# Optimization experiments

Hardware: AMD Instinct MI355X
Metric: run time of the kernel (lower is better)

Reference implementation:

```python
import jax, jax.numpy as jnp
import numpy as np

EPS = 1e-6
DELTA = 1e-6
GAMMA = 1.0


def setup_inputs() -> dict:
    key = jax.random.key(0)
    ks = jax.random.split(key, 6)
    B, N, D, DDIR, DSIM = 2, 384, 256, 128, 64
    sc = lambda d: 1.0 / np.sqrt(d)
    return {
        "t": jax.random.normal(ks[0], (B, N, D), jnp.float32),
        "Qd": jax.random.normal(ks[1], (D, DDIR), jnp.float32) * sc(D),
        "Kd": jax.random.normal(ks[2], (D, DDIR), jnp.float32) * sc(D),
        "Vd": jax.random.normal(ks[3], (DDIR, D), jnp.float32) * sc(DDIR),
        "Qs": jax.random.normal(ks[4], (D, DSIM), jnp.float32) * sc(D),
        "Ks": jax.random.normal(ks[5], (D, DSIM), jnp.float32) * sc(D),
        "a_l": jnp.ones((1,), jnp.float32),
        "b_l": jnp.zeros((1,), jnp.float32),
    }


def reference(t, Qd, Kd, Vd, Qs, Ks, a_l, b_l):
    B, N, D = t.shape
    d_sim = Qs.shape[1]
    # --- similarity: s_ij = <Qs t_i, Ks t_j>/sqrt(d_sim), then symmetrize ---
    q = t @ Qs  # (B,N,d_sim)
    k = t @ Ks
    s = jnp.einsum('bnd,bmd->bnm', q, k) / jnp.sqrt(jnp.float32(d_sim))
    s = 0.5 * (s + s.transpose(0, 2, 1))
    # --- global z-score over off-diagonal entries (biased var) ---
    eye = jnp.eye(N, dtype=bool)[None]  # (1,N,N)
    cnt = jnp.float32(N * (N - 1))
    mu = jnp.where(eye, 0.0, s).sum((1, 2), keepdims=True) / cnt  # (B,1,1)
    var = jnp.where(eye, 0.0, (s - mu) ** 2).sum((1, 2), keepdims=True) / cnt
    s_hat = (s - mu) / jnp.sqrt(var + EPS)
    tilde_s = a_l.reshape(-1, 1, 1) * s_hat + b_l.reshape(-1, 1, 1)
    # --- gates / mass / inertia / apportioned step ---
    A = jax.nn.sigmoid(tilde_s)                                  # (B,N,N)
    m = 1.0 / (jnp.exp(GAMMA * tilde_s).sum(axis=2) + EPS)       # (B,N)
    w = A * m[:, None, :]                                        # w_ij = m_j A_ij
    alpha = A * (w / (w.sum(axis=2, keepdims=True) + DELTA))     # (B,N,N)
    # --- antisymmetric Hadamard direction gate ---
    qd = t @ Qd  # (B,N,d_dir)
    kd = t @ Kd
    had = qd[:, :, None, :] * kd[:, None, :, :]                  # (B,N,N,d_dir)
    kappa = jnp.einsum('bijr,rd->bijd', had, Vd)                 # (B,N,N,D)
    gate = jax.nn.sigmoid(kappa - kappa.transpose(0, 2, 1, 3))
    Dpair = gate * (t[:, :, None, :] - t[:, None, :, :])         # D_ij = gate*(t_i - t_j)
    # --- exclude self pairs, aggregate update ---
    off = ~eye  # (1,N,N)
    alpha = jnp.where(off, alpha, 0.0)
    Dpair = jnp.where(off[..., None], Dpair, 0.0)
    t_next = t - jnp.einsum('bnm,bnmd->bnd', alpha, Dpair)
    return t_next
```

## Files before the change

### kernel.cpp

```cpp
#include <hip/hip_runtime.h>

#define Bn 2
#define Nn 384
#define Dn 256
#define Rn 128
#define Sn 64
#define BNn (Bn*Nn)

typedef short short8 __attribute__((ext_vector_type(8)));
typedef float f32x4 __attribute__((ext_vector_type(4)));
typedef unsigned int uint;
typedef unsigned short ushort;

static __device__ __forceinline__ float fast_sigmoid(float x) {
    return __builtin_amdgcn_rcpf(1.0f + __expf(-x));
}

static __device__ __forceinline__ ushort f2bf(float f) {
    uint u = __float_as_uint(f);
    uint r = (u + 0x7fffu + ((u >> 16) & 1u)) >> 16;
    return (ushort)r;
}
static __device__ __forceinline__ float bf2f(ushort u) {
    return __uint_as_float(((uint)u) << 16);
}

__global__ void zero_stats(float* __restrict__ stats) {
    if (threadIdx.x < 8) stats[threadIdx.x] = 0.0f;
}

__global__ void proj_kernel(const float* __restrict__ t,
                            const float* __restrict__ Qd, const float* __restrict__ Kd,
                            const float* __restrict__ Qs, const float* __restrict__ Ks,
                            float* __restrict__ q, float* __restrict__ k,
                            ushort* __restrict__ qdb, ushort* __restrict__ kdb) {
    __shared__ float trow[4][Dn];
    const int r0 = blockIdx.x * 4;
    const int tid = threadIdx.x;
    for (int idx = tid; idx < 4 * Dn; idx += 384)
        trow[idx >> 8][idx & 255] = t[(size_t)(r0 + (idx >> 8)) * Dn + (idx & 255)];
    __syncthreads();
    const float* W;
    float* of = nullptr;
    ushort* ob = nullptr;
    int ncol, col;
    if (tid < 64)       { W = Qs; of = q;   ncol = 64;  col = tid; }
    else if (tid < 128) { W = Ks; of = k;   ncol = 64;  col = tid - 64; }
    else if (tid < 256) { W = Qd; ob = qdb; ncol = 128; col = tid - 128; }
    else                { W = Kd; ob = kdb; ncol = 128; col = tid - 256; }
    float a0 = 0.f, a1 = 0.f, a2 = 0.f, a3 = 0.f;
    for (int kk = 0; kk < Dn; kk += 4) {
        float4 t0 = *(const float4*)&trow[0][kk];
        float4 t1 = *(const float4*)&trow[1][kk];
        float4 t2 = *(const float4*)&trow[2][kk];
        float4 t3 = *(const float4*)&trow[3][kk];
        float w0 = W[(size_t)(kk + 0) * ncol + col];
        float w1 = W[(size_t)(kk + 1) * ncol + col];
        float w2 = W[(size_t)(kk + 2) * ncol + col];
        float w3 = W[(size_t)(kk + 3) * ncol + col];
        a0 += t0.x * w0 + t0.y * w1 + t0.z * w2 + t0.w * w3;
        a1 += t1.x * w0 + t1.y * w1 + t1.z * w2 + t1.w * w3;
        a2 += t2.x * w0 + t2.y * w1 + t2.z * w2 + t2.w * w3;
        a3 += t3.x * w0 + t3.y * w1 + t3.z * w2 + t3.w * w3;
    }
    if (of) {
        of[(size_t)(r0 + 0) * ncol + col] = a0;
        of[(size_t)(r0 + 1) * ncol + col] = a1;
        of[(size_t)(r0 + 2) * ncol + col] = a2;
        of[(size_t)(r0 + 3) * ncol + col] = a3;
    } else {
        ob[(size_t)(r0 + 0) * ncol + col] = f2bf(a0);
        ob[(size_t)(r0 + 1) * ncol + col] = f2bf(a1);
        ob[(size_t)(r0 + 2) * ncol + col] = f2bf(a2);
        ob[(size_t)(r0 + 3) * ncol + col] = f2bf(a3);
    }
}

__global__ void prep_vdt(const float* __restrict__ Vd, ushort* __restrict__ VdT) {
    const int idx = blockIdx.x * 256 + threadIdx.x;
    const int d = idx >> 7, r = idx & 127;
    VdT[idx] = f2bf(Vd[(size_t)r * Dn + d]);
}

__global__ void ssym_kernel(const float* __restrict__ q, const float* __restrict__ k,
                            float* __restrict__ ssym, float* __restrict__ stats) {
    __shared__ float qi[16][68], ki[16][68], qj[16][68], kj[16][68];
    __shared__ float red[256];
    const int b = blockIdx.z, it = blockIdx.x, jt = blockIdx.y;
    const int tid = threadIdx.x;
    const int r0 = tid >> 6, c = tid & 63;
#pragma unroll
    for (int p = 0; p < 4; ++p) {
        int row = r0 + 4 * p;
        qi[row][c] = q[((size_t)(b * Nn + it * 16 + row)) * Sn + c];
        ki[row][c] = k[((size_t)(b * Nn + it * 16 + row)) * Sn + c];
        qj[row][c] = q[((size_t)(b * Nn + jt * 16 + row)) * Sn + c];
        kj[row][c] = k[((size_t)(b * Nn + jt * 16 + row)) * Sn + c];
    }
    __syncthreads();
    const int ti = tid >> 4, tj = tid & 15;
    float acc = 0.0f;
#pragma unroll
    for (int dd = 0; dd < Sn; dd += 4) {
        float4 a  = *(const float4*)&qi[ti][dd];
        float4 bb = *(const float4*)&kj[tj][dd];
        float4 cc = *(const float4*)&qj[tj][dd];
        float4 d  = *(const float4*)&ki[ti][dd];
        acc += a.x * bb.x + a.y * bb.y + a.z * bb.z + a.w * bb.w
             + cc.x * d.x + cc.y * d.y + cc.z * d.z + cc.w * d.w;
    }
    const float sval = acc * 0.0625f;
    const int gi = it * 16 + ti, gj = jt * 16 + tj;
    ssym[((size_t)(b * Nn + gi)) * Nn + gj] = sval;
    const float v = (gi == gj) ? 0.0f : sval;

    red[tid] = v;
    __syncthreads();
    for (int off = 128; off > 0; off >>= 1) {
        if (tid < off) red[tid] += red[tid + off];
        __syncthreads();
    }
    const float tot_s = red[0];
    __syncthreads();
    red[tid] = v * v;
    __syncthreads();
    for (int off = 128; off > 0; off >>= 1) {
        if (tid < off) red[tid] += red[tid + off];
        __syncthreads();
    }
    if (tid == 0) {
        atomicAdd(&stats[b * 2 + 0], tot_s);
        atomicAdd(&stats[b * 2 + 1], red[0]);
    }
}

__global__ void stats_fin(float* __restrict__ stats) {
    const int b = threadIdx.x;
    if (b < Bn) {
        const float cnt = (float)(Nn * (Nn - 1));
        const float mu = stats[b * 2 + 0] / cnt;
        const float var = stats[b * 2 + 1] / cnt - mu * mu;
        stats[4 + b * 2 + 0] = mu;
        stats[4 + b * 2 + 1] = rsqrtf(var + 1e-6f);
    }
}

__global__ void m_kernel(const float* __restrict__ ssym, const float* __restrict__ stats,
                         const float* __restrict__ a_l, const float* __restrict__ b_l,
                         float* __restrict__ m) {
    const int row = blockIdx.x;
    const int b = row / Nn;
    const float mu = stats[4 + b * 2], isg = stats[5 + b * 2];
    const float a = a_l[0], bb = b_l[0];
    const int tid = threadIdx.x;
    float sum = 0.0f;
    for (int j = tid; j < Nn; j += 128) {
        float til = a * (ssym[(size_t)row * Nn + j] - mu) * isg + bb;
        sum += __expf(til);
    }
    __shared__ float red[128];
    red[tid] = sum;
    __syncthreads();
    for (int off = 64; off > 0; off >>= 1) {
        if (tid < off) red[tid] += red[tid + off];
        __syncthreads();
    }
    if (tid == 0) m[row] = 1.0f / (red[0] + 1e-6f);
}

__global__ void alpha_kernel(const float* __restrict__ ssym, const float* __restrict__ stats,
                             const float* __restrict__ a_l, const float* __restrict__ b_l,
                             const float* __restrict__ m, float* __restrict__ alpha) {
    const int row = blockIdx.x;
    const int b = row / Nn;
    const int i = row - b * Nn;
    const float mu = stats[4 + b * 2], isg = stats[5 + b * 2];
    const float a = a_l[0], bb = b_l[0];
    const int tid = threadIdx.x;
    float wsum = 0.0f;
    for (int j = tid; j < Nn; j += 128) {
        float til = a * (ssym[(size_t)row * Nn + j] - mu) * isg + bb;
        float A = fast_sigmoid(til);
        wsum += A * m[b * Nn + j];
    }
    __shared__ float red[128];
    red[tid] = wsum;
    __syncthreads();
    for (int off = 64; off > 0; off >>= 1) {
        if (tid < off) red[tid] += red[tid + off];
        __syncthreads();
    }
    const float inv = 1.0f / (red[0] + 1e-6f);
    for (int j = tid; j < Nn; j += 128) {
        float til = a * (ssym[(size_t)row * Nn + j] - mu) * isg + bb;
        float A = fast_sigmoid(til);
        float al = A * A * m[b * Nn + j] * inv;
        alpha[(size_t)row * Nn + j] = (j == i) ? 0.0f : al;
    }
}

__global__ __launch_bounds__(256, 3)
void pair_kernel(const float* __restrict__ t, const ushort* __restrict__ qdb,
                 const ushort* __restrict__ kdb, const ushort* __restrict__ VdT,
                 const float* __restrict__ alpha, float* __restrict__ out) {
    __shared__ ushort h_s[128][136];
    __shared__ float alpha_s[Nn];
    __shared__ float qdi_s[Rn], kdi_s[Rn];

    const int bi = blockIdx.x;
    const int b = bi / Nn;
    const int tid = threadIdx.x;
    const int wave = tid >> 6, lane = tid & 63;
    const int ln = lane & 15, quad = lane >> 4;
    const int wd0 = wave * 64;

    for (int idx = tid; idx < Nn; idx += 256) alpha_s[idx] = alpha[(size_t)bi * Nn + idx];
    if (tid < Rn) {
        qdi_s[tid] = bf2f(qdb[(size_t)bi * Rn + tid]);
        kdi_s[tid] = bf2f(kdb[(size_t)bi * Rn + tid]);
    }

    short8 vf[4][4];
#pragma unroll
    for (int dt = 0; dt < 4; ++dt)
#pragma unroll
        for (int ks = 0; ks < 4; ++ks)
            vf[dt][ks] = *(const short8*)&VdT[(size_t)(wd0 + dt * 16 + ln) * Rn + ks * 32 + quad * 8];

    float4 tiv[4];
#pragma unroll
    for (int dt = 0; dt < 4; ++dt)
        tiv[dt] = *(const float4*)&t[(size_t)bi * Dn + wd0 + dt * 16 + quad * 4];

    float4 outac[4];
#pragma unroll
    for (int dt = 0; dt < 4; ++dt) outac[dt] = make_float4(0.f, 0.f, 0.f, 0.f);

    __syncthreads();

    for (int jt0 = 0; jt0 < Nn; jt0 += 128) {
        {
            const int jj = tid >> 1;
            const int r0 = (tid & 1) * 64;
            const size_t rowj = (size_t)(b * Nn + jt0 + jj) * Rn;
            const uint4* qp = (const uint4*)(qdb + rowj + r0);
            const uint4* kp = (const uint4*)(kdb + rowj + r0);
#pragma unroll
            for (int c = 0; c < 8; ++c) {
                uint4 qv = qp[c], kv = kp[c];
                uint pk[4];
#pragma unroll
                for (int p = 0; p < 4; ++p) {
                    uint qu = (&qv.x)[p], ku = (&kv.x)[p];
                    float qlo = __uint_as_float(qu << 16);
                    float qhi = __uint_as_float(qu & 0xffff0000u);
                    float klo = __uint_as_float(ku << 16);
                    float khi = __uint_as_float(ku & 0xffff0000u);
                    const int r = r0 + c * 8 + p * 2;
                    float h0 = qdi_s[r]     * klo - kdi_s[r]     * qlo;
                    float h1 = qdi_s[r + 1] * khi - kdi_s[r + 1] * qhi;
                    pk[p] = (uint)f2bf(h0) | ((uint)f2bf(h1) << 16);
                }
                uint4 w; w.x = pk[0]; w.y = pk[1]; w.z = pk[2]; w.w = pk[3];
                *(uint4*)&h_s[jj][r0 + c * 8] = w;
            }
        }
        __syncthreads();

#pragma unroll 1
        for (int jsub = 0; jsub < 8; ++jsub) {
            short8 hf[4];
#pragma unroll
            for (int ks = 0; ks < 4; ++ks)
                hf[ks] = *(const short8*)&h_s[jsub * 16 + ln][ks * 32 + quad * 8];
            const int j = jt0 + jsub * 16 + ln;
            const float al = alpha_s[j];
            const size_t trow = (size_t)(b * Nn + j) * Dn;
#pragma unroll
            for (int dt = 0; dt < 4; ++dt) {
                float4 tj = *(const float4*)&t[trow + wd0 + dt * 16 + quad * 4];
                f32x4 acc = {0.f, 0.f, 0.f, 0.f};
#pragma unroll
                for (int ks = 0; ks < 4; ++ks)
                    acc = __builtin_amdgcn_mfma_f32_16x16x32_bf16(vf[dt][ks], hf[ks], acc, 0, 0, 0);
                outac[dt].x += al * fast_sigmoid(acc[0]) * (tiv[dt].x - tj.x);
                outac[dt].y += al * fast_sigmoid(acc[1]) * (tiv[dt].y - tj.y);
                outac[dt].z += al * fast_sigmoid(acc[2]) * (tiv[dt].z - tj.z);
                outac[dt].w += al * fast_sigmoid(acc[3]) * (tiv[dt].w - tj.w);
            }
        }
        __syncthreads();
    }

#pragma unroll
    for (int dt = 0; dt < 4; ++dt) {
        float4 v = outac[dt];
#pragma unroll
        for (int mask = 1; mask < 16; mask <<= 1) {
            v.x += __shfl_xor(v.x, mask);
            v.y += __shfl_xor(v.y, mask);
            v.z += __shfl_xor(v.z, mask);
            v.w += __shfl_xor(v.w, mask);
        }
        if (ln == 0) {
            float4 o;
            o.x = tiv[dt].x - v.x;
            o.y = tiv[dt].y - v.y;
            o.z = tiv[dt].z - v.z;
            o.w = tiv[dt].w - v.w;
            *(float4*)&out[(size_t)bi * Dn + wd0 + dt * 16 + quad * 4] = o;
        }
    }
}

extern "C" void kernel_launch(void* const* d_in, const int* in_sizes, int n_in,
                              void* d_out, int out_size, void* d_ws, size_t ws_size,
                              hipStream_t stream) {
    const float* t   = (const float*)d_in[0];
    const float* Qd  = (const float*)d_in[1];
    const float* Kd  = (const float*)d_in[2];
    const float* Vd  = (const float*)d_in[3];
    const float* Qs  = (const float*)d_in[4];
    const float* Ks  = (const float*)d_in[5];
    const float* a_l = (const float*)d_in[6];
    const float* b_l = (const float*)d_in[7];
    float* out = (float*)d_out;
    float* ws  = (float*)d_ws;

    float* q     = ws;
    float* k     = q + BNn * Sn;
    float* ssym  = k + BNn * Sn;
    float* alpha = ssym + (size_t)BNn * Nn;
    float* m     = alpha + (size_t)BNn * Nn;
    float* stats = m + BNn;
    ushort* qdb  = (ushort*)(stats + 8);
    ushort* kdb  = qdb + (size_t)BNn * Rn;
    ushort* VdT  = kdb + (size_t)BNn * Rn;

    hipLaunchKernelGGL(zero_stats, dim3(1), dim3(64), 0, stream, stats);
    hipLaunchKernelGGL(proj_kernel, dim3(BNn / 4), dim3(384), 0, stream,
                       t, Qd, Kd, Qs, Ks, q, k, qdb, kdb);
    hipLaunchKernelGGL(prep_vdt, dim3(128), dim3(256), 0, stream, Vd, VdT);
    hipLaunchKernelGGL(ssym_kernel, dim3(Nn / 16, Nn / 16, Bn), dim3(256), 0, stream,
                       q, k, ssym, stats);
    hipLaunchKernelGGL(stats_fin, dim3(1), dim3(64), 0, stream, stats);
    hipLaunchKernelGGL(m_kernel, dim3(BNn), dim3(128), 0, stream, ssym, stats, a_l, b_l, m);
    hipLaunchKernelGGL(alpha_kernel, dim3(BNn), dim3(128), 0, stream, ssym, stats, a_l, b_l, m, alpha);
    hipLaunchKernelGGL(pair_kernel, dim3(BNn), dim3(256), 0, stream,
                       t, qdb, kdb, VdT, alpha, out);
}
```

Measured before the change: 197.7 us.

## Fuse prep and alpha kernels, fold log2e into Vd, split MFMA chains

Merges the stats zeroing, projection and Vd transpose kernels into one prep kernel, and folds the stats finalisation and alpha computation into the m and pair kernels. This cuts the launch count and drops the alpha buffer round-trip through global memory. It also pre-scales VdT by -log2(e) so the gate sigmoid uses exp2 directly. In the pair kernel, t_j loads are hoisted ahead of the MFMAs and the dependent MFMA chain is split into two independent accumulators. In exchange, every pair block recomputes its alpha row and the stats finalisation.

```diff
diff --git a/kernel.cpp b/kernel.cpp
--- a/kernel.cpp
+++ b/kernel.cpp
@@ -6,6 +6,7 @@
 #define Rn 128
 #define Sn 64
 #define BNn (Bn*Nn)
+#define NEG_LOG2E -1.44269504088896f
 
 typedef short short8 __attribute__((ext_vector_type(8)));
 typedef float f32x4 __attribute__((ext_vector_type(4)));
@@ -15,7 +16,6 @@
 static __device__ __forceinline__ float fast_sigmoid(float x) {
     return __builtin_amdgcn_rcpf(1.0f + __expf(-x));
 }
-
 static __device__ __forceinline__ ushort f2bf(float f) {
     uint u = __float_as_uint(f);
     uint r = (u + 0x7fffu + ((u >> 16) & 1u)) >> 16;
@@ -25,65 +25,81 @@
     return __uint_as_float(((uint)u) << 16);
 }
 
-__global__ void zero_stats(float* __restrict__ stats) {
-    if (threadIdx.x < 8) stats[threadIdx.x] = 0.0f;
-}
-
-__global__ void proj_kernel(const float* __restrict__ t,
-                            const float* __restrict__ Qd, const float* __restrict__ Kd,
-                            const float* __restrict__ Qs, const float* __restrict__ Ks,
-                            float* __restrict__ q, float* __restrict__ k,
-                            ushort* __restrict__ qdb, ushort* __restrict__ kdb) {
+__global__ __launch_bounds__(256)
+void prep_kernel(const float* __restrict__ t,
+                 const float* __restrict__ Qd, const float* __restrict__ Kd,
+                 const float* __restrict__ Vd,
+                 const float* __restrict__ Qs, const float* __restrict__ Ks,
+                 float* __restrict__ q, float* __restrict__ k,
+                 ushort* __restrict__ qdb, ushort* __restrict__ kdb,
+                 ushort* __restrict__ VdT, float* __restrict__ stats) {
+    const int bi = blockIdx.x;
+    const int tid = threadIdx.x;
+    if (bi >= 192) {
+        const int idx = (bi - 192) * 256 + tid;
+        const int d = idx >> 7, r = idx & 127;
+        VdT[idx] = f2bf(NEG_LOG2E * Vd[(size_t)r * Dn + d]);
+        if (bi == 319 && tid < 4) stats[tid] = 0.0f;
+        return;
+    }
     __shared__ float trow[4][Dn];
-    const int r0 = blockIdx.x * 4;
-    const int tid = threadIdx.x;
-    for (int idx = tid; idx < 4 * Dn; idx += 384)
-        trow[idx >> 8][idx & 255] = t[(size_t)(r0 + (idx >> 8)) * Dn + (idx & 255)];
-    __syncthreads();
-    const float* W;
-    float* of = nullptr;
-    ushort* ob = nullptr;
-    int ncol, col;
-    if (tid < 64)       { W = Qs; of = q;   ncol = 64;  col = tid; }
-    else if (tid < 128) { W = Ks; of = k;   ncol = 64;  col = tid - 64; }
-    else if (tid < 256) { W = Qd; ob = qdb; ncol = 128; col = tid - 128; }
-    else                { W = Kd; ob = kdb; ncol = 128; col = tid - 256; }
-    float a0 = 0.f, a1 = 0.f, a2 = 0.f, a3 = 0.f;
-    for (int kk = 0; kk < Dn; kk += 4) {
-        float4 t0 = *(const float4*)&trow[0][kk];
-        float4 t1 = *(const float4*)&trow[1][kk];
-        float4 t2 = *(const float4*)&trow[2][kk];
-        float4 t3 = *(const float4*)&trow[3][kk];
-        float w0 = W[(size_t)(kk + 0) * ncol + col];
-        float w1 = W[(size_t)(kk + 1) * ncol + col];
-        float w2 = W[(size_t)(kk + 2) * ncol + col];
-        float w3 = W[(size_t)(kk + 3) * ncol + col];
-        a0 += t0.x * w0 + t0.y * w1 + t0.z * w2 + t0.w * w3;
-        a1 += t1.x * w0 + t1.y * w1 + t1.z * w2 + t1.w * w3;
-        a2 += t2.x * w0 + t2.y * w1 + t2.z * w2 + t2.w * w3;
-        a3 += t3.x * w0 + t3.y * w1 + t3.z * w2 + t3.w * w3;
-    }
-    if (of) {
-        of[(size_t)(r0 + 0) * ncol + col] = a0;
-        of[(size_t)(r0 + 1) * ncol + col] = a1;
-        of[(size_t)(r0 + 2) * ncol + col] = a2;
-        of[(size_t)(r0 + 3) * ncol + col] = a3;
-    } else {
-        ob[(size_t)(r0 + 0) * ncol + col] = f2bf(a0);
-        ob[(size_t)(r0 + 1) * ncol + col] = f2bf(a1);
-        ob[(size_t)(r0 + 2) * ncol + col] = f2bf(a2);
-        ob[(size_t)(r0 + 3) * ncol + col] = f2bf(a3);
-    }
-}
-
-__global__ void prep_vdt(const float* __restrict__ Vd, ushort* __restrict__ VdT) {
-    const int idx = blockIdx.x * 256 + threadIdx.x;
-    const int d = idx >> 7, r = idx & 127;
-    VdT[idx] = f2bf(Vd[(size_t)r * Dn + d]);
-}
-
-__global__ void ssym_kernel(const float* __restrict__ q, const float* __restrict__ k,
-                            float* __restrict__ ssym, float* __restrict__ stats) {
+    const int r0 = bi * 4;
+    for (int idx = tid; idx < 4 * Dn; idx += 256)
+        trow[idx >> 8][idx & 255] = t[(size_t)r0 * Dn + idx];
+    __syncthreads();
+    {
+        const float* W = (tid < 128) ? Qd : Kd;
+        ushort* ob = (tid < 128) ? qdb : kdb;
+        const int col = tid & 127;
+        float a0 = 0.f, a1 = 0.f, a2 = 0.f, a3 = 0.f;
+        for (int kk = 0; kk < Dn; kk += 4) {
+            float4 t0 = *(const float4*)&trow[0][kk];
+            float4 t1 = *(const float4*)&trow[1][kk];
+            float4 t2 = *(const float4*)&trow[2][kk];
+            float4 t3 = *(const float4*)&trow[3][kk];
+            float w0 = W[(size_t)(kk + 0) * 128 + col];
+            float w1 = W[(size_t)(kk + 1) * 128 + col];
+            float w2 = W[(size_t)(kk + 2) * 128 + col];
+            float w3 = W[(size_t)(kk + 3) * 128 + col];
+            a0 += t0.x * w0 + t0.y * w1 + t0.z * w2 + t0.w * w3;
+            a1 += t1.x * w0 + t1.y * w1 + t1.z * w2 + t1.w * w3;
+            a2 += t2.x * w0 + t2.y * w1 + t2.z * w2 + t2.w * w3;
+            a3 += t3.x * w0 + t3.y * w1 + t3.z * w2 + t3.w * w3;
+        }
+        ob[(size_t)(r0 + 0) * 128 + col] = f2bf(a0);
+        ob[(size_t)(r0 + 1) * 128 + col] = f2bf(a1);
+        ob[(size_t)(r0 + 2) * 128 + col] = f2bf(a2);
+        ob[(size_t)(r0 + 3) * 128 + col] = f2bf(a3);
+    }
+    if (tid < 128) {
+        const float* W = (tid < 64) ? Qs : Ks;
+        float* of = (tid < 64) ? q : k;
+        const int col = tid & 63;
+        float a0 = 0.f, a1 = 0.f, a2 = 0.f, a3 = 0.f;
+        for (int kk = 0; kk < Dn; kk += 4) {
+            float4 t0 = *(const float4*)&trow[0][kk];
+            float4 t1 = *(const float4*)&trow[1][kk];
+            float4 t2 = *(const float4*)&trow[2][kk];
+            float4 t3 = *(const float4*)&trow[3][kk];
+            float w0 = W[(size_t)(kk + 0) * 64 + col];
+            float w1 = W[(size_t)(kk + 1) * 64 + col];
+            float w2 = W[(size_t)(kk + 2) * 64 + col];
+            float w3 = W[(size_t)(kk + 3) * 64 + col];
+            a0 += t0.x * w0 + t0.y * w1 + t0.z * w2 + t0.w * w3;
+            a1 += t1.x * w0 + t1.y * w1 + t1.z * w2 + t1.w * w3;
+            a2 += t2.x * w0 + t2.y * w1 + t2.z * w2 + t2.w * w3;
+            a3 += t3.x * w0 + t3.y * w1 + t3.z * w2 + t3.w * w3;
+        }
+        of[(size_t)(r0 + 0) * 64 + col] = a0;
+        of[(size_t)(r0 + 1) * 64 + col] = a1;
+        of[(size_t)(r0 + 2) * 64 + col] = a2;
+        of[(size_t)(r0 + 3) * 64 + col] = a3;
+    }
+}
+
+__global__ __launch_bounds__(256)
+void ssym_kernel(const float* __restrict__ q, const float* __restrict__ k,
+                 float* __restrict__ ssym, float* __restrict__ stats) {
     __shared__ float qi[16][68], ki[16][68], qj[16][68], kj[16][68];
     __shared__ float red[256];
     const int b = blockIdx.z, it = blockIdx.x, jt = blockIdx.y;
@@ -134,87 +150,78 @@
     }
 }
 
-__global__ void stats_fin(float* __restrict__ stats) {
-    const int b = threadIdx.x;
-    if (b < Bn) {
-        const float cnt = (float)(Nn * (Nn - 1));
-        const float mu = stats[b * 2 + 0] / cnt;
-        const float var = stats[b * 2 + 1] / cnt - mu * mu;
-        stats[4 + b * 2 + 0] = mu;
-        stats[4 + b * 2 + 1] = rsqrtf(var + 1e-6f);
-    }
-}
-
-__global__ void m_kernel(const float* __restrict__ ssym, const float* __restrict__ stats,
-                         const float* __restrict__ a_l, const float* __restrict__ b_l,
-                         float* __restrict__ m) {
+__global__ __launch_bounds__(256)
+void m_kernel(const float* __restrict__ ssym, const float* __restrict__ stats,
+              const float* __restrict__ a_l, const float* __restrict__ b_l,
+              float* __restrict__ m) {
+    __shared__ float red[256];
     const int row = blockIdx.x;
     const int b = row / Nn;
-    const float mu = stats[4 + b * 2], isg = stats[5 + b * 2];
-    const float a = a_l[0], bb = b_l[0];
+    const float cnt_inv = 1.0f / (float)(Nn * (Nn - 1));
+    const float mu = stats[b * 2 + 0] * cnt_inv;
+    const float var = stats[b * 2 + 1] * cnt_inv - mu * mu;
+    const float isg = rsqrtf(var + 1e-6f);
+    const float a = a_l[0], bbias = b_l[0];
     const int tid = threadIdx.x;
-    float sum = 0.0f;
-    for (int j = tid; j < Nn; j += 128) {
-        float til = a * (ssym[(size_t)row * Nn + j] - mu) * isg + bb;
-        sum += __expf(til);
-    }
-    __shared__ float red[128];
+    float sum = __expf(a * (ssym[(size_t)row * Nn + tid] - mu) * isg + bbias);
+    if (tid < 128)
+        sum += __expf(a * (ssym[(size_t)row * Nn + 256 + tid] - mu) * isg + bbias);
     red[tid] = sum;
     __syncthreads();
-    for (int off = 64; off > 0; off >>= 1) {
+    for (int off = 128; off > 0; off >>= 1) {
         if (tid < off) red[tid] += red[tid + off];
         __syncthreads();
     }
     if (tid == 0) m[row] = 1.0f / (red[0] + 1e-6f);
 }
 
-__global__ void alpha_kernel(const float* __restrict__ ssym, const float* __restrict__ stats,
-                             const float* __restrict__ a_l, const float* __restrict__ b_l,
-                             const float* __restrict__ m, float* __restrict__ alpha) {
-    const int row = blockIdx.x;
-    const int b = row / Nn;
-    const int i = row - b * Nn;
-    const float mu = stats[4 + b * 2], isg = stats[5 + b * 2];
-    const float a = a_l[0], bb = b_l[0];
-    const int tid = threadIdx.x;
-    float wsum = 0.0f;
-    for (int j = tid; j < Nn; j += 128) {
-        float til = a * (ssym[(size_t)row * Nn + j] - mu) * isg + bb;
-        float A = fast_sigmoid(til);
-        wsum += A * m[b * Nn + j];
-    }
-    __shared__ float red[128];
-    red[tid] = wsum;
-    __syncthreads();
-    for (int off = 64; off > 0; off >>= 1) {
-        if (tid < off) red[tid] += red[tid + off];
-        __syncthreads();
-    }
-    const float inv = 1.0f / (red[0] + 1e-6f);
-    for (int j = tid; j < Nn; j += 128) {
-        float til = a * (ssym[(size_t)row * Nn + j] - mu) * isg + bb;
-        float A = fast_sigmoid(til);
-        float al = A * A * m[b * Nn + j] * inv;
-        alpha[(size_t)row * Nn + j] = (j == i) ? 0.0f : al;
-    }
-}
-
 __global__ __launch_bounds__(256, 3)
-void pair_kernel(const float* __restrict__ t, const ushort* __restrict__ qdb,
-                 const ushort* __restrict__ kdb, const ushort* __restrict__ VdT,
-                 const float* __restrict__ alpha, float* __restrict__ out) {
+void pair_kernel(const float* __restrict__ t, const float* __restrict__ ssym,
+                 const float* __restrict__ mptr, const float* __restrict__ stats,
+                 const float* __restrict__ a_l, const float* __restrict__ b_l,
+                 const ushort* __restrict__ qdb, const ushort* __restrict__ kdb,
+                 const ushort* __restrict__ VdT, float* __restrict__ out) {
     __shared__ ushort h_s[128][136];
     __shared__ float alpha_s[Nn];
     __shared__ float qdi_s[Rn], kdi_s[Rn];
+    __shared__ float red[256];
 
     const int bi = blockIdx.x;
     const int b = bi / Nn;
+    const int i = bi - b * Nn;
     const int tid = threadIdx.x;
     const int wave = tid >> 6, lane = tid & 63;
     const int ln = lane & 15, quad = lane >> 4;
     const int wd0 = wave * 64;
 
-    for (int idx = tid; idx < Nn; idx += 256) alpha_s[idx] = alpha[(size_t)bi * Nn + idx];
+    {
+        const float cnt_inv = 1.0f / (float)(Nn * (Nn - 1));
+        const float mu = stats[b * 2 + 0] * cnt_inv;
+        const float var = stats[b * 2 + 1] * cnt_inv - mu * mu;
+        const float isg = rsqrtf(var + 1e-6f);
+        const float a = a_l[0], bbias = b_l[0];
+        float A0, am0, A1 = 0.f, am1 = 0.f;
+        {
+            float s0 = ssym[(size_t)bi * Nn + tid];
+            A0 = fast_sigmoid(a * (s0 - mu) * isg + bbias);
+            am0 = A0 * mptr[b * Nn + tid];
+        }
+        if (tid < 128) {
+            float s1 = ssym[(size_t)bi * Nn + 256 + tid];
+            A1 = fast_sigmoid(a * (s1 - mu) * isg + bbias);
+            am1 = A1 * mptr[b * Nn + 256 + tid];
+        }
+        red[tid] = am0 + am1;
+        __syncthreads();
+        for (int off = 128; off > 0; off >>= 1) {
+            if (tid < off) red[tid] += red[tid + off];
+            __syncthreads();
+        }
+        const float inv = 1.0f / (red[0] + 1e-6f);
+        alpha_s[tid] = (tid == i) ? 0.f : A0 * am0 * inv;
+        if (tid < 128)
+            alpha_s[256 + tid] = ((256 + tid) == i) ? 0.f : A1 * am1 * inv;
+    }
     if (tid < Rn) {
         qdi_s[tid] = bf2f(qdb[(size_t)bi * Rn + tid]);
         kdi_s[tid] = bf2f(kdb[(size_t)bi * Rn + tid]);
@@ -236,15 +243,14 @@
 #pragma unroll
     for (int dt = 0; dt < 4; ++dt) outac[dt] = make_float4(0.f, 0.f, 0.f, 0.f);
 
-    __syncthreads();
-
     for (int jt0 = 0; jt0 < Nn; jt0 += 128) {
+        __syncthreads();
         {
             const int jj = tid >> 1;
-            const int r0 = (tid & 1) * 64;
+            const int r0s = (tid & 1) * 64;
             const size_t rowj = (size_t)(b * Nn + jt0 + jj) * Rn;
-            const uint4* qp = (const uint4*)(qdb + rowj + r0);
-            const uint4* kp = (const uint4*)(kdb + rowj + r0);
+            const uint4* qp = (const uint4*)(qdb + rowj + r0s);
+            const uint4* kp = (const uint4*)(kdb + rowj + r0s);
 #pragma unroll
             for (int c = 0; c < 8; ++c) {
                 uint4 qv = qp[c], kv = kp[c];
@@ -256,13 +262,13 @@
                     float qhi = __uint_as_float(qu & 0xffff0000u);
                     float klo = __uint_as_float(ku << 16);
                     float khi = __uint_as_float(ku & 0xffff0000u);
-                    const int r = r0 + c * 8 + p * 2;
+                    const int r = r0s + c * 8 + p * 2;
                     float h0 = qdi_s[r]     * klo - kdi_s[r]     * qlo;
                     float h1 = qdi_s[r + 1] * khi - kdi_s[r + 1] * qhi;
                     pk[p] = (uint)f2bf(h0) | ((uint)f2bf(h1) << 16);
                 }
                 uint4 w; w.x = pk[0]; w.y = pk[1]; w.z = pk[2]; w.w = pk[3];
-                *(uint4*)&h_s[jj][r0 + c * 8] = w;
+                *(uint4*)&h_s[jj][r0s + c * 8] = w;
             }
         }
         __syncthreads();
@@ -275,21 +281,39 @@
                 hf[ks] = *(const short8*)&h_s[jsub * 16 + ln][ks * 32 + quad * 8];
             const int j = jt0 + jsub * 16 + ln;
             const float al = alpha_s[j];
-            const size_t trow = (size_t)(b * Nn + j) * Dn;
+            const size_t trow_ = (size_t)(b * Nn + j) * Dn;
+            float4 tjv[4];
+#pragma unroll
+            for (int dt = 0; dt < 4; ++dt)
+                tjv[dt] = *(const float4*)&t[trow_ + wd0 + dt * 16 + quad * 4];
+
+            f32x4 aA[4], aB[4];
 #pragma unroll
             for (int dt = 0; dt < 4; ++dt) {
-                float4 tj = *(const float4*)&t[trow + wd0 + dt * 16 + quad * 4];
-                f32x4 acc = {0.f, 0.f, 0.f, 0.f};
-#pragma unroll
-                for (int ks = 0; ks < 4; ++ks)
-                    acc = __builtin_amdgcn_mfma_f32_16x16x32_bf16(vf[dt][ks], hf[ks], acc, 0, 0, 0);
-                outac[dt].x += al * fast_sigmoid(acc[0]) * (tiv[dt].x - tj.x);
-                outac[dt].y += al * fast_sigmoid(acc[1]) * (tiv[dt].y - tj.y);
-                outac[dt].z += al * fast_sigmoid(acc[2]) * (tiv[dt].z - tj.z);
-                outac[dt].w += al * fast_sigmoid(acc[3]) * (tiv[dt].w - tj.w);
+                f32x4 x = {0.f, 0.f, 0.f, 0.f}, y = {0.f, 0.f, 0.f, 0.f};
+                x = __builtin_amdgcn_mfma_f32_16x16x32_bf16(vf[dt][0], hf[0], x, 0, 0, 0);
+                y = __builtin_amdgcn_mfma_f32_16x16x32_bf16(vf[dt][1], hf[1], y, 0, 0, 0);
+                x = __builtin_amdgcn_mfma_f32_16x16x32_bf16(vf[dt][2], hf[2], x, 0, 0, 0);
+                y = __builtin_amdgcn_mfma_f32_16x16x32_bf16(vf[dt][3], hf[3], y, 0, 0, 0);
+                aA[dt] = x; aB[dt] = y;
             }
-        }
-        __syncthreads();
+#pragma unroll
+            for (int dt = 0; dt < 4; ++dt) {
+                const float4 tj = tjv[dt];
+                float e0 = aA[dt][0] + aB[dt][0];
+                float e1 = aA[dt][1] + aB[dt][1];
+                float e2 = aA[dt][2] + aB[dt][2];
+                float e3 = aA[dt][3] + aB[dt][3];
+                float g0 = __builtin_amdgcn_rcpf(1.0f + __builtin_amdgcn_exp2f(e0));
+                float g1 = __builtin_amdgcn_rcpf(1.0f + __builtin_amdgcn_exp2f(e1));
+                float g2 = __builtin_amdgcn_rcpf(1.0f + __builtin_amdgcn_exp2f(e2));
+                float g3 = __builtin_amdgcn_rcpf(1.0f + __builtin_amdgcn_exp2f(e3));
+                outac[dt].x += al * g0 * (tiv[dt].x - tj.x);
+                outac[dt].y += al * g1 * (tiv[dt].y - tj.y);
+                outac[dt].z += al * g2 * (tiv[dt].z - tj.z);
+                outac[dt].w += al * g3 * (tiv[dt].w - tj.w);
+            }
+        }
     }
 
 #pragma unroll
@@ -330,22 +354,17 @@
     float* q     = ws;
     float* k     = q + BNn * Sn;
     float* ssym  = k + BNn * Sn;
-    float* alpha = ssym + (size_t)BNn * Nn;
-    float* m     = alpha + (size_t)BNn * Nn;
+    float* m     = ssym + (size_t)BNn * Nn;
     float* stats = m + BNn;
     ushort* qdb  = (ushort*)(stats + 8);
     ushort* kdb  = qdb + (size_t)BNn * Rn;
     ushort* VdT  = kdb + (size_t)BNn * Rn;
 
-    hipLaunchKernelGGL(zero_stats, dim3(1), dim3(64), 0, stream, stats);
-    hipLaunchKernelGGL(proj_kernel, dim3(BNn / 4), dim3(384), 0, stream,
-                       t, Qd, Kd, Qs, Ks, q, k, qdb, kdb);
-    hipLaunchKernelGGL(prep_vdt, dim3(128), dim3(256), 0, stream, Vd, VdT);
+    hipLaunchKernelGGL(prep_kernel, dim3(320), dim3(256), 0, stream,
+                       t, Qd, Kd, Vd, Qs, Ks, q, k, qdb, kdb, VdT, stats);
     hipLaunchKernelGGL(ssym_kernel, dim3(Nn / 16, Nn / 16, Bn), dim3(256), 0, stream,
                        q, k, ssym, stats);
-    hipLaunchKernelGGL(stats_fin, dim3(1), dim3(64), 0, stream, stats);
-    hipLaunchKernelGGL(m_kernel, dim3(BNn), dim3(128), 0, stream, ssym, stats, a_l, b_l, m);
-    hipLaunchKernelGGL(alpha_kernel, dim3(BNn), dim3(128), 0, stream, ssym, stats, a_l, b_l, m, alpha);
+    hipLaunchKernelGGL(m_kernel, dim3(BNn), dim3(256), 0, stream, ssym, stats, a_l, b_l, m);
     hipLaunchKernelGGL(pair_kernel, dim3(BNn), dim3(256), 0, stream,
-                       t, qdb, kdb, VdT, alpha, out);
-}
+                       t, ssym, m, stats, a_l, b_l, qdb, kdb, VdT, out);
+}
```

Measured after the change: 187.2 us. 5.3% less time.
